# Kernel tuning notes

Measured on AMD Instinct MI355X. Metric: run time of the kernel, lower is better.

Reference implementation:

```python
import jax, jax.numpy as jnp
import numpy as np

T, B, E, H = 2048, 2, 1024, 16
D = E // H
NEG = -1e18


def setup_inputs() -> dict:
    key = jax.random.key(0)
    k1, k2, k3, k4, k5 = jax.random.split(key, 5)
    return {
        "query": jax.random.normal(k1, (T, B, E), dtype=jnp.float32),
        "in_proj_weight": jax.random.normal(k2, (3 * E, E), dtype=jnp.float32) * 0.02,
        "in_proj_bias": jax.random.normal(k3, (3 * E,), dtype=jnp.float32) * 0.02,
        "out_proj_weight": jax.random.normal(k4, (E, E), dtype=jnp.float32) * 0.02,
        "out_proj_bias": jax.random.normal(k5, (E,), dtype=jnp.float32) * 0.02,
    }


def reference(query, in_proj_weight, in_proj_bias, out_proj_weight, out_proj_bias):
    # Self-attention (qkv_same), mask_future_timesteps=True, no padding mask,
    # eval mode (dropout p=0), need_weights=True.
    tgt_len, bsz, embed_dim = query.shape
    # fused in-projection: [T,B,3E]
    qkv = jnp.einsum("tbe,fe->tbf", query, in_proj_weight) + in_proj_bias
    q, k, v = jnp.split(qkv, 3, axis=-1)
    q = q * (D ** -0.5)
    # [T,B,E] -> [B*H, T, D]
    def to_heads(x):
        return x.reshape(tgt_len, bsz * H, D).transpose(1, 0, 2)
    q, k, v = to_heads(q), to_heads(k), to_heads(v)
    # scores: [B*H, T, T]
    scores = jnp.einsum("ntd,nsd->nts", q, k)
    causal = jnp.triu(jnp.full((tgt_len, tgt_len), NEG, dtype=scores.dtype), k=1)
    scores = scores + causal[None, :, :]
    attn_weights = jax.nn.softmax(scores, axis=-1)
    # context: [B*H, T, D] -> [T, B, E]
    ctx = jnp.einsum("nts,nsd->ntd", attn_weights, v)
    ctx = ctx.transpose(1, 0, 2).reshape(tgt_len, bsz, embed_dim)
    out = jnp.einsum("tbe,fe->tbf", ctx, out_proj_weight) + out_proj_bias
    # averaged attention weights over heads: [B, T, T]
    avg_w = attn_weights.reshape(bsz, H, tgt_len, tgt_len).sum(axis=1) / H
    return (out, avg_w)
```

## Files before the change

### kernel.cpp

```cpp
#include <hip/hip_runtime.h>
#include <math.h>

#define T_LEN 2048
#define BSZ 2
#define EMB 1024
#define NHEAD 16
#define HDIM 64
#define QK_LD 2048

typedef __attribute__((ext_vector_type(8))) short short8v;
typedef __attribute__((ext_vector_type(4))) float floatx4;

__device__ __forceinline__ short f2bf(float f) {
    unsigned u = __float_as_uint(f);
    u += 0x7fffu + ((u >> 16) & 1u);
    return (short)(u >> 16);
}

__device__ __forceinline__ void async16(const short* g, short* l) {
    __builtin_amdgcn_global_load_lds(
        (const __attribute__((address_space(1))) void*)g,
        (__attribute__((address_space(3))) void*)l, 16, 0, 0);
}

__global__ __launch_bounds__(256) void f32_to_bf16_k(const float* __restrict__ src,
                                                     short* __restrict__ dst, int n) {
    int i = (blockIdx.x * 256 + threadIdx.x) * 4;
    if (i >= n) return;
    float4 v = *(const float4*)(src + i);
    short4 o = make_short4(f2bf(v.x), f2bf(v.y), f2bf(v.z), f2bf(v.w));
    *(short4*)(dst + i) = o;
}

__global__ __launch_bounds__(256) void gemm_bf16(const short* __restrict__ A,
        const short* __restrict__ B, const float* __restrict__ bias,
        void* __restrict__ Cout, short* __restrict__ vTout,
        int M, int N, int K, int scale_cols, int out_bf16, int ldC) {
    __shared__ short As[128][32];
    __shared__ short Bs[128][32];
    const int tid = threadIdx.x;
    const int m0 = blockIdx.x * 128, n0 = blockIdx.y * 128;
    const int lane = tid & 63, w = tid >> 6;
    const int q = lane >> 4, r = lane & 15;
    const int wr = w >> 1, wc = w & 1;

    const int srow = lane >> 2;
    const int spos = lane & 3;
    const int rowL = w * 16 + srow;
    const int rowH = 64 + rowL;
    const int csrc = spos ^ ((rowL >> 1) & 3);
    const short* gA0 = A + (size_t)(m0 + rowL) * K + csrc * 8;
    const short* gA1 = A + (size_t)(m0 + rowH) * K + csrc * 8;
    const short* gB0 = B + (size_t)(n0 + rowL) * K + csrc * 8;
    const short* gB1 = B + (size_t)(n0 + rowH) * K + csrc * 8;
    short* lA0 = &As[w * 16][0];
    short* lA1 = &As[64 + w * 16][0];
    short* lB0 = &Bs[w * 16][0];
    short* lB1 = &Bs[64 + w * 16][0];

    floatx4 acc[4][4];
    #pragma unroll
    for (int a = 0; a < 4; ++a)
        #pragma unroll
        for (int b2 = 0; b2 < 4; ++b2)
            #pragma unroll
            for (int e = 0; e < 4; ++e) acc[a][b2][e] = 0.f;

    for (int k0 = 0; k0 < K; k0 += 32) {
        __syncthreads();
        async16(gA0 + k0, lA0);
        async16(gA1 + k0, lA1);
        async16(gB0 + k0, lB0);
        async16(gB1 + k0, lB1);
        __syncthreads();
        short8v af[4], bfr[4];
        #pragma unroll
        for (int mb = 0; mb < 4; ++mb) {
            int row = wr * 64 + mb * 16 + r;
            af[mb] = *(const short8v*)&As[row][(q ^ ((row >> 1) & 3)) * 8];
        }
        #pragma unroll
        for (int nb = 0; nb < 4; ++nb) {
            int row = wc * 64 + nb * 16 + r;
            bfr[nb] = *(const short8v*)&Bs[row][(q ^ ((row >> 1) & 3)) * 8];
        }
        #pragma unroll
        for (int mb = 0; mb < 4; ++mb)
            #pragma unroll
            for (int nb = 0; nb < 4; ++nb)
                acc[mb][nb] = __builtin_amdgcn_mfma_f32_16x16x32_bf16(af[mb], bfr[nb], acc[mb][nb], 0, 0, 0);
    }

    #pragma unroll
    for (int nb = 0; nb < 4; ++nb) {
        const int col = n0 + wc * 64 + nb * 16 + r;
        const float bi = bias[col];
        const float sc = (col < scale_cols) ? 0.125f : 1.0f;
        if (vTout && col >= 2 * EMB) {
            const int e = col - 2 * EMB;
            #pragma unroll
            for (int mb = 0; mb < 4; ++mb) {
                const int base = m0 + wr * 64 + mb * 16 + q * 4;
                float v0 = acc[mb][nb][0] + bi, v1 = acc[mb][nb][1] + bi;
                float v2 = acc[mb][nb][2] + bi, v3 = acc[mb][nb][3] + bi;
                unsigned lo = (unsigned short)f2bf(v0) | ((unsigned)(unsigned short)f2bf(v2) << 16);
                unsigned hi = (unsigned short)f2bf(v1) | ((unsigned)(unsigned short)f2bf(v3) << 16);
                *(unsigned*)&vTout[(size_t)e * T_LEN + (base >> 1)]         = lo;
                *(unsigned*)&vTout[((size_t)EMB + e) * T_LEN + (base >> 1)] = hi;
            }
        } else {
            #pragma unroll
            for (int mb = 0; mb < 4; ++mb)
                #pragma unroll
                for (int i = 0; i < 4; ++i) {
                    const int rowg = m0 + wr * 64 + mb * 16 + q * 4 + i;
                    const float v = (acc[mb][nb][i] + bi) * sc;
                    if (out_bf16) ((short*)Cout)[(size_t)rowg * ldC + col] = f2bf(v);
                    else          ((float*)Cout)[(size_t)rowg * ldC + col] = v;
                }
        }
    }
}

__global__ __launch_bounds__(256) void flash_fwd(const short* __restrict__ qk,
        const short* __restrict__ vT, short* __restrict__ ctx,
        float* __restrict__ Lr) {
    __shared__ short Ks[128][64];
    __shared__ short Vt[64][128];
    __shared__ short Ps[2][64][64];
    __shared__ float Lred[4][64];
    const int tid = threadIdx.x;
    const int bh = blockIdx.x;
    const int tt = 31 - blockIdx.y;
    const int t0 = tt << 6;
    const int b = bh >> 4, h = bh & 15;
    const int lane = tid & 63, w = tid >> 6;
    const int q = lane >> 4, r = lane & 15;
    const int RS = BSZ * QK_LD;

    const short* qbase = qk + (size_t)b * QK_LD + h * HDIM;
    const short* kbase = qbase + EMB;
    const short* vbase = vT + ((size_t)b * EMB + h * HDIM) * T_LEN;

    const int krow0 = w * 32 + (lane >> 3);
    const short* kg = kbase + (size_t)krow0 * RS + ((lane & 7) ^ (krow0 & 7)) * 8;
    const int vrow0 = w * 16 + (lane >> 4);
    const short* vg[4];
    #pragma unroll
    for (int j = 0; j < 4; ++j) {
        const int vr = vrow0 + j * 4;
        const int gc = ((lane & 15) & 8) | (((lane & 15) & 7) ^ (vr & 7));
        vg[j] = vbase + (size_t)vr * T_LEN + gc * 8;
    }

    {
        const int sr = tid >> 3, c8 = tid & 7;
        *(int4*)&Ps[0][sr][(c8 ^ (sr & 7)) * 8] =
            *(const int4*)(qbase + (size_t)(t0 + sr) * RS + c8 * 8);
        *(int4*)&Ps[0][sr + 32][(c8 ^ ((sr + 32) & 7)) * 8] =
            *(const int4*)(qbase + (size_t)(t0 + sr + 32) * RS + c8 * 8);
    }
    __syncthreads();
    short8v qf[4][2];
    #pragma unroll
    for (int mb = 0; mb < 4; ++mb)
        #pragma unroll
        for (int ks = 0; ks < 2; ++ks) {
            int row = mb * 16 + r;
            qf[mb][ks] = *(const short8v*)&Ps[0][row][((ks * 4 + q) ^ (row & 7)) * 8];
        }

    float l_part[4][4];
    floatx4 o[4];
    #pragma unroll
    for (int mb = 0; mb < 4; ++mb)
        #pragma unroll
        for (int i = 0; i < 4; ++i) l_part[mb][i] = 0.f;
    #pragma unroll
    for (int nb = 0; nb < 4; ++nb)
        #pragma unroll
        for (int e = 0; e < 4; ++e) o[nb][e] = 0.f;

    const int ntiles = tt + 1;
    int s2 = 0;
    for (; s2 + 2 <= ntiles; s2 += 2) {
        __syncthreads();
        {
            const short* kgr = kg + (size_t)(s2 * 64) * RS;
            #pragma unroll
            for (int j = 0; j < 4; ++j)
                async16(kgr + (size_t)(j * 8) * RS, &Ks[w * 32 + j * 8][0]);
            #pragma unroll
            for (int j = 0; j < 4; ++j)
                async16(vg[j] + s2 * 64, &Vt[w * 16 + j * 4][0]);
        }
        __syncthreads();
        #pragma unroll
        for (int t2 = 0; t2 < 2; ++t2) {
            floatx4 sf[4];
            #pragma unroll
            for (int mb = 0; mb < 4; ++mb)
                #pragma unroll
                for (int e = 0; e < 4; ++e) sf[mb][e] = 0.f;
            #pragma unroll
            for (int ks = 0; ks < 2; ++ks) {
                const int krow = t2 * 64 + w * 16 + r;
                short8v kf = *(const short8v*)&Ks[krow][((ks * 4 + q) ^ (krow & 7)) * 8];
                #pragma unroll
                for (int mb = 0; mb < 4; ++mb)
                    sf[mb] = __builtin_amdgcn_mfma_f32_16x16x32_bf16(qf[mb][ks], kf, sf[mb], 0, 0, 0);
            }
            const bool diag = (s2 + t2 == tt);
            #pragma unroll
            for (int mb = 0; mb < 4; ++mb)
                #pragma unroll
                for (int i = 0; i < 4; ++i) {
                    const int rl = mb * 16 + q * 4 + i;
                    float p = (diag && (w * 16 + r > rl)) ? 0.f : __expf(sf[mb][i]);
                    l_part[mb][i] += p;
                    const int c = (w * 2 + (r >> 3)) ^ (rl & 7);
                    Ps[t2][rl][c * 8 + (r & 7)] = f2bf(p);
                }
        }
        __syncthreads();
        #pragma unroll
        for (int ks = 0; ks < 2; ++ks) {
            const int prow = w * 16 + r;
            const int pcp = ((ks * 4 + q) ^ (prow & 7)) * 8;
            short8v pfA = *(const short8v*)&Ps[0][prow][pcp];
            short8v pfB = *(const short8v*)&Ps[1][prow][pcp];
            #pragma unroll
            for (int nb = 0; nb < 4; ++nb) {
                const int vrow = nb * 16 + r;
                const int pcv = (ks * 4 + q) ^ (vrow & 7);
                short8v vfA = *(const short8v*)&Vt[vrow][pcv * 8];
                short8v vfB = *(const short8v*)&Vt[vrow][(8 | pcv) * 8];
                o[nb] = __builtin_amdgcn_mfma_f32_16x16x32_bf16(pfA, vfA, o[nb], 0, 0, 0);
                o[nb] = __builtin_amdgcn_mfma_f32_16x16x32_bf16(pfB, vfB, o[nb], 0, 0, 0);
            }
        }
    }
    if (s2 < ntiles) {
        __syncthreads();
        {
            const int sr = tid >> 2, cb = (tid & 3) * 2;
            const short* kp = kbase + (size_t)(s2 * 64 + sr) * RS;
            const short* vp = vbase + (size_t)sr * T_LEN + s2 * 64;
            #pragma unroll
            for (int u = 0; u < 2; ++u) {
                const int c = cb + u;
                *(int4*)&Ks[sr][(c ^ (sr & 7)) * 8] = *(const int4*)(kp + c * 8);
                *(int4*)&Vt[sr][(c ^ (sr & 7)) * 8] = *(const int4*)(vp + c * 8);
            }
        }
        __syncthreads();
        floatx4 sf[4];
        #pragma unroll
        for (int mb = 0; mb < 4; ++mb)
            #pragma unroll
            for (int e = 0; e < 4; ++e) sf[mb][e] = 0.f;
        #pragma unroll
        for (int ks = 0; ks < 2; ++ks) {
            const int krow = w * 16 + r;
            short8v kf = *(const short8v*)&Ks[krow][((ks * 4 + q) ^ (krow & 7)) * 8];
            #pragma unroll
            for (int mb = 0; mb < 4; ++mb)
                sf[mb] = __builtin_amdgcn_mfma_f32_16x16x32_bf16(qf[mb][ks], kf, sf[mb], 0, 0, 0);
        }
        #pragma unroll
        for (int mb = 0; mb < 4; ++mb)
            #pragma unroll
            for (int i = 0; i < 4; ++i) {
                const int rl = mb * 16 + q * 4 + i;
                float p = (w * 16 + r > rl) ? 0.f : __expf(sf[mb][i]);
                l_part[mb][i] += p;
                const int c = (w * 2 + (r >> 3)) ^ (rl & 7);
                Ps[0][rl][c * 8 + (r & 7)] = f2bf(p);
            }
        __syncthreads();
        #pragma unroll
        for (int ks = 0; ks < 2; ++ks) {
            const int prow = w * 16 + r;
            short8v pf = *(const short8v*)&Ps[0][prow][((ks * 4 + q) ^ (prow & 7)) * 8];
            #pragma unroll
            for (int nb = 0; nb < 4; ++nb) {
                const int vrow = nb * 16 + r;
                short8v vf = *(const short8v*)&Vt[vrow][(((ks * 4 + q) ^ (vrow & 7))) * 8];
                o[nb] = __builtin_amdgcn_mfma_f32_16x16x32_bf16(pf, vf, o[nb], 0, 0, 0);
            }
        }
    }

    #pragma unroll
    for (int mb = 0; mb < 4; ++mb)
        #pragma unroll
        for (int i = 0; i < 4; ++i) {
            float v = l_part[mb][i];
            v += __shfl_xor(v, 1, 16);
            v += __shfl_xor(v, 2, 16);
            v += __shfl_xor(v, 4, 16);
            v += __shfl_xor(v, 8, 16);
            if (r == 0) Lred[w][mb * 16 + q * 4 + i] = v;
        }
    __syncthreads();
    if (tid < 64) {
        float s = Lred[0][tid] + Lred[1][tid] + Lred[2][tid] + Lred[3][tid];
        Lr[(size_t)bh * T_LEN + t0 + tid] = s;
        Lred[0][tid] = s;
    }
    __syncthreads();
    #pragma unroll
    for (int i = 0; i < 4; ++i) {
        const int tl = w * 16 + q * 4 + i;
        const float inv = 1.0f / Lred[0][tl];
        #pragma unroll
        for (int nb = 0; nb < 4; ++nb)
            ctx[((size_t)(t0 + tl) * BSZ + b) * EMB + h * HDIM + nb * 16 + r] =
                f2bf(o[nb][i] * inv);
    }
}

__global__ __launch_bounds__(256) void avg_w_k(const short* __restrict__ qk,
        const float* __restrict__ Lr, float* __restrict__ avg) {
    const int s0 = blockIdx.x * 64, t0 = blockIdx.y * 64, b = blockIdx.z;
    const int tid = threadIdx.x;
    float* outb = avg + (size_t)b * T_LEN * T_LEN;
    if (s0 > t0) {
        const int ty = tid >> 4, tx = tid & 15;
        const float4 z = make_float4(0.f, 0.f, 0.f, 0.f);
        #pragma unroll
        for (int i = 0; i < 4; ++i)
            *(float4*)&outb[(size_t)(t0 + ty * 4 + i) * T_LEN + s0 + tx * 4] = z;
        return;
    }
    __shared__ short Qs[64][128];
    __shared__ short Ks[64][128];
    __shared__ float Lbuf[NHEAD][64];
    const int lane = tid & 63, w = tid >> 6;
    const int q = lane >> 4, r = lane & 15;
    const int srow = tid >> 2, c4 = (tid & 3) * 4;
    const short* qbase = qk + (size_t)b * QK_LD;
    const int RS = BSZ * QK_LD;

    #pragma unroll
    for (int u = 0; u < 4; ++u) {
        const int li = tid * 4 + u;
        const int h = li >> 6, tl = li & 63;
        Lbuf[h][tl] = 0.0625f / Lr[(size_t)(b * NHEAD + h) * T_LEN + t0 + tl];
    }

    floatx4 acc[4];
    #pragma unroll
    for (int nb = 0; nb < 4; ++nb)
        #pragma unroll
        for (int e = 0; e < 4; ++e) acc[nb][e] = 0.f;

    for (int hp = 0; hp < 8; ++hp) {
        const short* qh = qbase + hp * 128;
        const short* kh = qbase + EMB + hp * 128;
        __syncthreads();
        #pragma unroll
        for (int u = 0; u < 4; ++u) {
            const int c = c4 + u;
            const int pc = (c & 8) | ((c & 7) ^ (srow & 7));
            *(int4*)&Qs[srow][pc * 8] =
                *(const int4*)(qh + (size_t)(t0 + srow) * RS + c * 8);
            *(int4*)&Ks[srow][pc * 8] =
                *(const int4*)(kh + (size_t)(s0 + srow) * RS + c * 8);
        }
        __syncthreads();

        #pragma unroll
        for (int hs = 0; hs < 2; ++hs) {
            const int h = hp * 2 + hs;
            floatx4 sf[4];
            #pragma unroll
            for (int nb = 0; nb < 4; ++nb)
                #pragma unroll
                for (int e = 0; e < 4; ++e) sf[nb][e] = 0.f;
            #pragma unroll
            for (int ks = 0; ks < 2; ++ks) {
                const int qrow = w * 16 + r;
                short8v qfr = *(const short8v*)
                    &Qs[qrow][((hs * 8) | ((ks * 4 + q) ^ (qrow & 7))) * 8];
                #pragma unroll
                for (int nb = 0; nb < 4; ++nb) {
                    const int krow = nb * 16 + r;
                    short8v kfr = *(const short8v*)
                        &Ks[krow][((hs * 8) | ((ks * 4 + q) ^ (krow & 7))) * 8];
                    sf[nb] = __builtin_amdgcn_mfma_f32_16x16x32_bf16(qfr, kfr, sf[nb], 0, 0, 0);
                }
            }
            #pragma unroll
            for (int i = 0; i < 4; ++i) {
                const int tl = w * 16 + q * 4 + i;
                const float inv = Lbuf[h][tl];
                #pragma unroll
                for (int nb = 0; nb < 4; ++nb) {
                    float e = (s0 == t0 && (nb * 16 + r > tl))
                              ? 0.f : __expf(sf[nb][i]) * inv;
                    acc[nb][i] += e;
                }
            }
        }
    }

    #pragma unroll
    for (int i = 0; i < 4; ++i) {
        const int t = t0 + w * 16 + q * 4 + i;
        #pragma unroll
        for (int nb = 0; nb < 4; ++nb)
            outb[(size_t)t * T_LEN + s0 + nb * 16 + r] = acc[nb][i];
    }
}

extern "C" void kernel_launch(void* const* d_in, const int* in_sizes, int n_in,
                              void* d_out, int out_size, void* d_ws, size_t ws_size,
                              hipStream_t stream) {
    (void)in_sizes; (void)n_in; (void)out_size; (void)ws_size;
    const float* query = (const float*)d_in[0];
    const float* w_in  = (const float*)d_in[1];
    const float* b_in  = (const float*)d_in[2];
    const float* w_out = (const float*)d_in[3];
    const float* b_out = (const float*)d_in[4];

    float* out = (float*)d_out;
    float* avg = out + (size_t)T_LEN * BSZ * EMB;

    short* ws     = (short*)d_ws;
    short* wb_in  = ws;
    short* wb_out = wb_in  + (size_t)3072 * 1024;
    short* qkb    = wb_out + (size_t)1024 * 1024;
    short* vTb    = qkb    + (size_t)4096 * 2048;
    short* ctxb   = vTb    + (size_t)BSZ * EMB * T_LEN;
    float* Lr     = (float*)(ctxb + (size_t)4096 * 1024);
    short* qb     = ctxb;

    f32_to_bf16_k<<<4096, 256, 0, stream>>>(query, qb,     4096 * 1024);
    f32_to_bf16_k<<<3072, 256, 0, stream>>>(w_in,  wb_in,  3072 * 1024);
    f32_to_bf16_k<<<1024, 256, 0, stream>>>(w_out, wb_out, 1024 * 1024);

    gemm_bf16<<<dim3(32, 24), 256, 0, stream>>>(qb, wb_in, b_in, qkb, vTb,
                                                4096, 3072, 1024, EMB, 1, QK_LD);
    flash_fwd<<<dim3(32, 32), 256, 0, stream>>>(qkb, vTb, ctxb, Lr);
    avg_w_k<<<dim3(32, 32, 2), 256, 0, stream>>>(qkb, Lr, avg);
    gemm_bf16<<<dim3(32, 8), 256, 0, stream>>>(ctxb, wb_out, b_out, out, (short*)0,
                                               4096, 1024, 1024, 0, 0, 1024);
}
```

Measured before the change: 244.1 us.

## Load avg_w MFMA fragments directly from global with register double-buffering

The avg_w kernel no longer stages Q and K tiles through shared memory with two barriers per head pair. Each lane now loads its MFMA fragments straight from global memory into registers, and the loads for the next head are issued before computing the current one (ping-pong buffering). This removes the LDS round-trip and the barriers. In exchange each wave re-reads K rows that other waves also read, relying on cache, and register pressure goes up.

```diff
diff --git a/kernel.cpp b/kernel.cpp
--- a/kernel.cpp
+++ b/kernel.cpp
@@ -333,14 +333,11 @@
             *(float4*)&outb[(size_t)(t0 + ty * 4 + i) * T_LEN + s0 + tx * 4] = z;
         return;
     }
-    __shared__ short Qs[64][128];
-    __shared__ short Ks[64][128];
     __shared__ float Lbuf[NHEAD][64];
     const int lane = tid & 63, w = tid >> 6;
     const int q = lane >> 4, r = lane & 15;
-    const int srow = tid >> 2, c4 = (tid & 3) * 4;
-    const short* qbase = qk + (size_t)b * QK_LD;
     const int RS = BSZ * QK_LD;
+    const bool diagblk = (s0 == t0);
 
     #pragma unroll
     for (int u = 0; u < 4; ++u) {
@@ -348,6 +345,13 @@
         const int h = li >> 6, tl = li & 63;
         Lbuf[h][tl] = 0.0625f / Lr[(size_t)(b * NHEAD + h) * T_LEN + t0 + tl];
     }
+    __syncthreads();
+
+    const short* qp = qk + (size_t)b * QK_LD + (size_t)(t0 + w * 16 + r) * RS + q * 8;
+    const short* kp0 = qk + (size_t)b * QK_LD + EMB + (size_t)(s0 + r) * RS + q * 8;
+    const short* kp[4];
+    #pragma unroll
+    for (int nb = 0; nb < 4; ++nb) kp[nb] = kp0 + (size_t)(nb * 16) * RS;
 
     floatx4 acc[4];
     #pragma unroll
@@ -355,55 +359,50 @@
         #pragma unroll
         for (int e = 0; e < 4; ++e) acc[nb][e] = 0.f;
 
-    for (int hp = 0; hp < 8; ++hp) {
-        const short* qh = qbase + hp * 128;
-        const short* kh = qbase + EMB + hp * 128;
-        __syncthreads();
-        #pragma unroll
-        for (int u = 0; u < 4; ++u) {
-            const int c = c4 + u;
-            const int pc = (c & 8) | ((c & 7) ^ (srow & 7));
-            *(int4*)&Qs[srow][pc * 8] =
-                *(const int4*)(qh + (size_t)(t0 + srow) * RS + c * 8);
-            *(int4*)&Ks[srow][pc * 8] =
-                *(const int4*)(kh + (size_t)(s0 + srow) * RS + c * 8);
-        }
-        __syncthreads();
-
-        #pragma unroll
-        for (int hs = 0; hs < 2; ++hs) {
-            const int h = hp * 2 + hs;
-            floatx4 sf[4];
-            #pragma unroll
-            for (int nb = 0; nb < 4; ++nb)
-                #pragma unroll
-                for (int e = 0; e < 4; ++e) sf[nb][e] = 0.f;
-            #pragma unroll
-            for (int ks = 0; ks < 2; ++ks) {
-                const int qrow = w * 16 + r;
-                short8v qfr = *(const short8v*)
-                    &Qs[qrow][((hs * 8) | ((ks * 4 + q) ^ (qrow & 7))) * 8];
-                #pragma unroll
-                for (int nb = 0; nb < 4; ++nb) {
-                    const int krow = nb * 16 + r;
-                    short8v kfr = *(const short8v*)
-                        &Ks[krow][((hs * 8) | ((ks * 4 + q) ^ (krow & 7))) * 8];
-                    sf[nb] = __builtin_amdgcn_mfma_f32_16x16x32_bf16(qfr, kfr, sf[nb], 0, 0, 0);
-                }
-            }
-            #pragma unroll
-            for (int i = 0; i < 4; ++i) {
-                const int tl = w * 16 + q * 4 + i;
-                const float inv = Lbuf[h][tl];
-                #pragma unroll
-                for (int nb = 0; nb < 4; ++nb) {
-                    float e = (s0 == t0 && (nb * 16 + r > tl))
-                              ? 0.f : __expf(sf[nb][i]) * inv;
-                    acc[nb][i] += e;
-                }
-            }
-        }
-    }
+#define LOADSET(Q0, Q1, KF, hh) do {                                         \
+        const int _off = (hh) * 64;                                          \
+        Q0 = *(const short8v*)(qp + _off);                                   \
+        Q1 = *(const short8v*)(qp + _off + 32);                              \
+        _Pragma("unroll")                                                    \
+        for (int _nb = 0; _nb < 4; ++_nb) {                                  \
+            KF[_nb * 2]     = *(const short8v*)(kp[_nb] + _off);             \
+            KF[_nb * 2 + 1] = *(const short8v*)(kp[_nb] + _off + 32);        \
+        }                                                                    \
+    } while (0)
+
+#define COMPUTE(Q0, Q1, KF, hh) do {                                         \
+        floatx4 sf[4];                                                       \
+        _Pragma("unroll")                                                    \
+        for (int _nb = 0; _nb < 4; ++_nb) {                                  \
+            _Pragma("unroll")                                                \
+            for (int _e = 0; _e < 4; ++_e) sf[_nb][_e] = 0.f;                \
+            sf[_nb] = __builtin_amdgcn_mfma_f32_16x16x32_bf16(Q0, KF[_nb * 2],     sf[_nb], 0, 0, 0); \
+            sf[_nb] = __builtin_amdgcn_mfma_f32_16x16x32_bf16(Q1, KF[_nb * 2 + 1], sf[_nb], 0, 0, 0); \
+        }                                                                    \
+        _Pragma("unroll")                                                    \
+        for (int _i = 0; _i < 4; ++_i) {                                     \
+            const int _tl = w * 16 + q * 4 + _i;                             \
+            const float _inv = Lbuf[hh][_tl];                                \
+            _Pragma("unroll")                                                \
+            for (int _nb = 0; _nb < 4; ++_nb) {                              \
+                float _e2 = (diagblk && (_nb * 16 + r > _tl))                \
+                            ? 0.f : __expf(sf[_nb][_i]) * _inv;              \
+                acc[_nb][_i] += _e2;                                         \
+            }                                                                \
+        }                                                                    \
+    } while (0)
+
+    short8v qA0, qA1, kA[8], qB0, qB1, kB[8];
+    LOADSET(qA0, qA1, kA, 0);
+    #pragma unroll
+    for (int h = 0; h < NHEAD; h += 2) {
+        LOADSET(qB0, qB1, kB, h + 1);
+        COMPUTE(qA0, qA1, kA, h);
+        if (h + 2 < NHEAD) LOADSET(qA0, qA1, kA, h + 2);
+        COMPUTE(qB0, qB1, kB, h + 1);
+    }
+#undef LOADSET
+#undef COMPUTE
 
     #pragma unroll
     for (int i = 0; i < 4; ++i) {
```

Result: slower. 338.9 us (+38.8%).
